# Performance work log

Hardware: AMD Instinct MI355X
Metric: run time of the kernel (lower is better)

The kernel has to match this reference:

```python
import jax, jax.numpy as jnp
import numpy as np

B, T, C = 2, 2048, 1024
H = 16
HS = C // H
EPS = 1e-5


def layernorm(x, g, b):
    mu = jnp.mean(x, axis=-1, keepdims=True)
    var = jnp.var(x, axis=-1, keepdims=True)
    return (x - mu) * jax.lax.rsqrt(var + EPS) * g + b


def setup_inputs() -> dict:
    key = jax.random.key(0)
    ks = jax.random.split(key, 12)
    s_in = 1.0 / np.sqrt(C)
    s_ff = 1.0 / np.sqrt(4 * C)
    return {
        "x": jax.random.normal(ks[0], (B, T, C), jnp.float32),
        "Wq": jax.random.normal(ks[1], (H, C, HS), jnp.float32) * s_in,
        "Wk": jax.random.normal(ks[2], (H, C, HS), jnp.float32) * s_in,
        "Wv": jax.random.normal(ks[3], (H, C, HS), jnp.float32) * s_in,
        "Wo": jax.random.normal(ks[4], (C, C), jnp.float32) * s_in,
        "bo": jnp.zeros((C,), jnp.float32),
        "W1": jax.random.normal(ks[5], (C, 4 * C), jnp.float32) * s_in,
        "b1": jnp.zeros((4 * C,), jnp.float32),
        "W2": jax.random.normal(ks[6], (4 * C, C), jnp.float32) * s_ff,
        "b2": jnp.zeros((C,), jnp.float32),
        "g1": jnp.ones((C,), jnp.float32),
        "be1": jnp.zeros((C,), jnp.float32),
        "g2": jnp.ones((C,), jnp.float32),
        "be2": jnp.zeros((C,), jnp.float32),
    }


def reference(x, Wq, Wk, Wv, Wo, bo, W1, b1, W2, b2, g1, be1, g2, be2):
    # x: [B,T,C]. Dropout is identity (eval mode).
    x = layernorm(x, g1, be1)
    # --- multi-head causal self-attention (per-source: scale by C**-0.5, NOT head_size) ---
    q = jnp.einsum("btc,hcd->bhtd", x, Wq)
    k = jnp.einsum("btc,hcd->bhtd", x, Wk)
    v = jnp.einsum("btc,hcd->bhtd", x, Wv)
    scores = jnp.einsum("bhtd,bhsd->bhts", q, k) * (C ** -0.5)  # [B,H,T,T]
    causal = jnp.tril(jnp.ones((T, T), bool))
    scores = jnp.where(causal, scores, -jnp.inf)
    wei = jax.nn.softmax(scores, axis=-1)
    attn = jnp.einsum("bhts,bhsd->bhtd", wei, v)
    attn = attn.transpose(0, 2, 1, 3).reshape(B, T, C)  # concat heads on last dim
    sa = attn @ Wo + bo
    x = x + sa
    # --- MLP with second pre-op LayerNorm ---
    x = layernorm(x, g2, be2)
    h = jax.nn.relu(x @ W1 + b1)
    x = x + (h @ W2 + b2)
    return x
```

## Files before the change

### kernel.cpp

```cpp
#include <hip/hip_runtime.h>
#include <hip/hip_bf16.h>
#include <math.h>

#define B_ 2
#define T_ 2048
#define C_ 1024
#define H_ 16
#define HS_ 64
#define N_ROWS (B_*T_)
#define MB (1024*1024)

typedef __attribute__((ext_vector_type(8))) short bf16x8;
typedef __attribute__((ext_vector_type(8))) unsigned short u16x8;
typedef __attribute__((ext_vector_type(4))) float floatx4;

static __device__ __forceinline__ unsigned short f2bf(float f) {
  union { float f; unsigned u; } v; v.f = f;
  unsigned r = v.u + 0x7fff + ((v.u >> 16) & 1);
  return (unsigned short)(r >> 16);
}
static __device__ __forceinline__ float bf2f(unsigned short s) {
  union { unsigned u; float f; } v; v.u = ((unsigned)s) << 16;
  return v.f;
}

__global__ __launch_bounds__(256) void ln_kernel(
    const float* __restrict__ x, const float* __restrict__ g,
    const float* __restrict__ b, unsigned short* __restrict__ outb)
{
  const int row = blockIdx.x;
  const int tid = threadIdx.x;
  const float* xr = x + (size_t)row * C_;
  float4 xv = *reinterpret_cast<const float4*>(xr + tid * 4);
  float s  = xv.x + xv.y + xv.z + xv.w;
  float ss = xv.x*xv.x + xv.y*xv.y + xv.z*xv.z + xv.w*xv.w;
  #pragma unroll
  for (int off = 32; off > 0; off >>= 1) {
    s  += __shfl_down(s, off, 64);
    ss += __shfl_down(ss, off, 64);
  }
  __shared__ float rs[4], rss[4];
  __shared__ float smu, srstd;
  if ((tid & 63) == 0) { rs[tid >> 6] = s; rss[tid >> 6] = ss; }
  __syncthreads();
  if (tid == 0) {
    float S  = rs[0] + rs[1] + rs[2] + rs[3];
    float SS = rss[0] + rss[1] + rss[2] + rss[3];
    float mu  = S * (1.0f / C_);
    float var = SS * (1.0f / C_) - mu * mu;
    smu = mu; srstd = rsqrtf(var + 1e-5f);
  }
  __syncthreads();
  const float mu = smu, rstd = srstd;
  float4 gv = *reinterpret_cast<const float4*>(g + tid * 4);
  float4 bv = *reinterpret_cast<const float4*>(b + tid * 4);
  union { unsigned long long ll; unsigned short s[4]; } o;
  o.s[0] = f2bf((xv.x - mu) * rstd * gv.x + bv.x);
  o.s[1] = f2bf((xv.y - mu) * rstd * gv.y + bv.y);
  o.s[2] = f2bf((xv.z - mu) * rstd * gv.z + bv.z);
  o.s[3] = f2bf((xv.w - mu) * rstd * gv.w + bv.w);
  *reinterpret_cast<unsigned long long*>(outb + (size_t)row * C_ + tid * 4) = o.ll;
}

__global__ __launch_bounds__(256) void transpose_cast(
    const float* __restrict__ in, unsigned short* __restrict__ out, int R, int Cc)
{
  __shared__ float tile[32][33];
  const int bz = blockIdx.z;
  in  += (size_t)bz * R * Cc;
  out += (size_t)bz * R * Cc;
  const int tx = threadIdx.x & 31;
  const int ty = threadIdx.x >> 5;
  const int c0 = blockIdx.x * 32, r0 = blockIdx.y * 32;
  #pragma unroll
  for (int j = 0; j < 4; ++j)
    tile[ty + j*8][tx] = in[(size_t)(r0 + ty + j*8) * Cc + c0 + tx];
  __syncthreads();
  #pragma unroll
  for (int j = 0; j < 4; ++j)
    out[(size_t)(c0 + ty + j*8) * R + r0 + tx] = f2bf(tile[tx][ty + j*8]);
}

__global__ __launch_bounds__(256) void transpose_cast_qkv(
    const float* __restrict__ Wq, const float* __restrict__ Wk,
    const float* __restrict__ Wv, unsigned short* __restrict__ out)
{
  __shared__ float tile[32][33];
  const int z = blockIdx.z;
  const int which = z >> 4, h = z & 15;
  const float* in = (which == 0 ? Wq : which == 1 ? Wk : Wv) + (size_t)h * C_ * HS_;
  unsigned short* dst = out + (size_t)z * C_ * HS_;
  const int tx = threadIdx.x & 31;
  const int ty = threadIdx.x >> 5;
  const int c0 = blockIdx.x * 32, r0 = blockIdx.y * 32;
  #pragma unroll
  for (int j = 0; j < 4; ++j)
    tile[ty + j*8][tx] = in[(size_t)(r0 + ty + j*8) * HS_ + c0 + tx];
  __syncthreads();
  #pragma unroll
  for (int j = 0; j < 4; ++j)
    dst[(size_t)(c0 + ty + j*8) * C_ + r0 + tx] = f2bf(tile[tx][ty + j*8]);
}

template<int TNB, bool OUTBF16, bool RELU, bool HASB, bool HASRES>
__global__ __launch_bounds__(256) void gemm_bf16(
    const unsigned short* __restrict__ A,
    const unsigned short* __restrict__ Bt,
    const float* __restrict__ bias,
    const unsigned short* __restrict__ res,
    void* __restrict__ Cout,
    int M, int N, int K)
{
  constexpr int NT = TNB / 32;
  constexpr int WN = TNB / 2;
  __shared__ unsigned short As[2][128 * 32];
  __shared__ unsigned short Bs[2][TNB * 32];
  const int tid  = threadIdx.x;
  const int lane = tid & 63;
  const int wave = tid >> 6;
  const int wm = wave & 1, wn = wave >> 1;
  const int m0 = blockIdx.x * 128, n0 = blockIdx.y * TNB;

  const int lrow = lane >> 2;
  const int lcol = (lane & 3) * 8;
  const int fr = lane & 15;
  const int fq = lane >> 4;

  floatx4 acc[4][NT] = {};

  const unsigned short* Aw = A  + (size_t)m0 * K;
  const unsigned short* Bw = Bt + (size_t)n0 * K;

  for (int k0 = 0; k0 < K; k0 += 64) {
    __syncthreads();
    #pragma unroll
    for (int half = 0; half < 2; ++half) {
      #pragma unroll
      for (int i = 0; i < 2; ++i) {
        const int rbase = i * 64 + wave * 16;
        const unsigned short* gp =
            Aw + (size_t)(rbase + lrow) * K + k0 + half * 32 + lcol;
        __builtin_amdgcn_global_load_lds(
            (const __attribute__((address_space(1))) void*)gp,
            (__attribute__((address_space(3))) void*)(As[half] + rbase * 32),
            16, 0, 0);
      }
      #pragma unroll
      for (int i = 0; i < TNB / 64; ++i) {
        const int rbase = i * 64 + wave * 16;
        const unsigned short* gp =
            Bw + (size_t)(rbase + lrow) * K + k0 + half * 32 + lcol;
        __builtin_amdgcn_global_load_lds(
            (const __attribute__((address_space(1))) void*)gp,
            (__attribute__((address_space(3))) void*)(Bs[half] + rbase * 32),
            16, 0, 0);
      }
    }
    __syncthreads();

    #pragma unroll
    for (int half = 0; half < 2; ++half) {
      bf16x8 af[4], bfr[NT];
      #pragma unroll
      for (int t = 0; t < 4; ++t)
        af[t]  = *reinterpret_cast<const bf16x8*>(
            As[half] + (wm*64 + t*16 + fr)*32 + fq*8);
      #pragma unroll
      for (int t = 0; t < NT; ++t)
        bfr[t] = *reinterpret_cast<const bf16x8*>(
            Bs[half] + (wn*WN + t*16 + fr)*32 + fq*8);
      #pragma unroll
      for (int mt = 0; mt < 4; ++mt)
        #pragma unroll
        for (int nt = 0; nt < NT; ++nt)
          acc[mt][nt] = __builtin_amdgcn_mfma_f32_16x16x32_bf16(
              af[mt], bfr[nt], acc[mt][nt], 0, 0, 0);
    }
  }

  #pragma unroll
  for (int nt = 0; nt < NT; ++nt) {
    const int col = n0 + wn*WN + nt*16 + fr;
    const float bv = HASB ? bias[col] : 0.0f;
    #pragma unroll
    for (int mt = 0; mt < 4; ++mt) {
      #pragma unroll
      for (int r = 0; r < 4; ++r) {
        const int row = m0 + wm*64 + mt*16 + fq*4 + r;
        float v = acc[mt][nt][r] + bv;
        if (RELU) v = v > 0.0f ? v : 0.0f;
        if (HASRES) v += bf2f(res[(size_t)row * N + col]);
        if (OUTBF16) ((unsigned short*)Cout)[(size_t)row * N + col] = f2bf(v);
        else         ((float*)Cout)[(size_t)row * N + col] = v;
      }
    }
  }
}

template<int TNB, int SPLITS>
__global__ __launch_bounds__(256) void gemm_splitk(
    const unsigned short* __restrict__ A,
    const unsigned short* __restrict__ Bt,
    unsigned short* __restrict__ Cpart,
    int M, int N, int Kfull)
{
  constexpr int NT = TNB / 32;
  constexpr int WN = TNB / 2;
  __shared__ unsigned short As[2][128 * 32];
  __shared__ unsigned short Bs[2][TNB * 32];
  const int tid  = threadIdx.x;
  const int lane = tid & 63;
  const int wave = tid >> 6;
  const int wm = wave & 1, wn = wave >> 1;
  const int m0 = blockIdx.x * 128, n0 = blockIdx.y * TNB;
  const int z  = blockIdx.z;
  const int Kh = Kfull / SPLITS;

  const int lrow = lane >> 2;
  const int lcol = (lane & 3) * 8;
  const int fr = lane & 15;
  const int fq = lane >> 4;

  floatx4 acc[4][NT] = {};

  const unsigned short* Aw = A  + (size_t)m0 * Kfull + (size_t)z * Kh;
  const unsigned short* Bw = Bt + (size_t)n0 * Kfull + (size_t)z * Kh;
  unsigned short* Cw = Cpart + (size_t)z * M * N;

  for (int k0 = 0; k0 < Kh; k0 += 64) {
    __syncthreads();
    #pragma unroll
    for (int half = 0; half < 2; ++half) {
      #pragma unroll
      for (int i = 0; i < 2; ++i) {
        const int rbase = i * 64 + wave * 16;
        const unsigned short* gp =
            Aw + (size_t)(rbase + lrow) * Kfull + k0 + half * 32 + lcol;
        __builtin_amdgcn_global_load_lds(
            (const __attribute__((address_space(1))) void*)gp,
            (__attribute__((address_space(3))) void*)(As[half] + rbase * 32),
            16, 0, 0);
      }
      #pragma unroll
      for (int i = 0; i < TNB / 64; ++i) {
        const int rbase = i * 64 + wave * 16;
        const unsigned short* gp =
            Bw + (size_t)(rbase + lrow) * Kfull + k0 + half * 32 + lcol;
        __builtin_amdgcn_global_load_lds(
            (const __attribute__((address_space(1))) void*)gp,
            (__attribute__((address_space(3))) void*)(Bs[half] + rbase * 32),
            16, 0, 0);
      }
    }
    __syncthreads();

    #pragma unroll
    for (int half = 0; half < 2; ++half) {
      bf16x8 af[4], bfr[NT];
      #pragma unroll
      for (int t = 0; t < 4; ++t)
        af[t]  = *reinterpret_cast<const bf16x8*>(
            As[half] + (wm*64 + t*16 + fr)*32 + fq*8);
      #pragma unroll
      for (int t = 0; t < NT; ++t)
        bfr[t] = *reinterpret_cast<const bf16x8*>(
            Bs[half] + (wn*WN + t*16 + fr)*32 + fq*8);
      #pragma unroll
      for (int mt = 0; mt < 4; ++mt)
        #pragma unroll
        for (int nt = 0; nt < NT; ++nt)
          acc[mt][nt] = __builtin_amdgcn_mfma_f32_16x16x32_bf16(
              af[mt], bfr[nt], acc[mt][nt], 0, 0, 0);
    }
  }

  #pragma unroll
  for (int nt = 0; nt < NT; ++nt) {
    const int col = n0 + wn*WN + nt*16 + fr;
    #pragma unroll
    for (int mt = 0; mt < 4; ++mt)
      #pragma unroll
      for (int r = 0; r < 4; ++r) {
        const int row = m0 + wm*64 + mt*16 + fq*4 + r;
        Cw[(size_t)row * N + col] = f2bf(acc[mt][nt][r]);
      }
  }
}

template<int SPLITS>
__global__ __launch_bounds__(256) void splitk_reduce(
    const unsigned short* __restrict__ p,
    const float* __restrict__ bias, const unsigned short* __restrict__ res,
    float* __restrict__ out)
{
  const size_t i = ((size_t)blockIdx.x * 256 + threadIdx.x) * 4;
  const size_t MN = (size_t)N_ROWS * C_;
  float4 bv = *reinterpret_cast<const float4*>(bias + (i & (size_t)(C_ - 1)));
  float acc[4] = {bv.x, bv.y, bv.z, bv.w};
  {
    const unsigned short* rp = res + i;
    #pragma unroll
    for (int j = 0; j < 4; ++j) acc[j] += bf2f(rp[j]);
  }
  #pragma unroll
  for (int z = 0; z < SPLITS; ++z) {
    const unsigned short* pp = p + (size_t)z * MN + i;
    #pragma unroll
    for (int j = 0; j < 4; ++j) acc[j] += bf2f(pp[j]);
  }
  float4 o; o.x = acc[0]; o.y = acc[1]; o.z = acc[2]; o.w = acc[3];
  *reinterpret_cast<float4*>(out + i) = o;
}

__global__ __launch_bounds__(256) void v_transpose(
    const unsigned short* __restrict__ qkv, unsigned short* __restrict__ vt)
{
  __shared__ __align__(16) unsigned short sT[64][72];
  const int st = blockIdx.x;
  const int bh = blockIdx.y;
  const int b = bh >> 4, h = bh & 15;
  const int t = threadIdx.x;
  const int r = t >> 2, c0 = (t & 3) * 16;
  const unsigned short* src =
      qkv + (size_t)(b * T_ + st * 64 + r) * 3072 + 2048 + h * 64 + c0;
  *(u16x8*)&sT[r][c0]     = *(const u16x8*)src;
  *(u16x8*)&sT[r][c0 + 8] = *(const u16x8*)(src + 8);
  __syncthreads();
  const int d = t >> 2, sc = (t & 3) * 16;
  unsigned short v[16];
  #pragma unroll
  for (int j = 0; j < 16; ++j) v[j] = sT[sc + j][d];
  unsigned short* dst = vt + ((size_t)bh * 64 + d) * (size_t)T_ + st * 64 + sc;
  *(uint4*)dst       = *(uint4*)&v[0];
  *(uint4*)(dst + 8) = *(uint4*)&v[8];
}

__global__ __launch_bounds__(256, 3) void attn_mfma(
    const unsigned short* __restrict__ qkv,
    const unsigned short* __restrict__ vt,
    unsigned short* __restrict__ out)
{
  const int bh = blockIdx.x;
  const int qt = (int)(gridDim.y - 1) - (int)blockIdx.y;
  const int b = bh >> 4, h = bh & 15;
  const int tid = threadIdx.x;
  const int w = tid >> 6;
  const int lane = tid & 63;
  const int l15 = lane & 15, fq = lane >> 4;
  const int t0 = qt * 64;
  const int q_row = t0 + w * 16 + l15;

  __shared__ __align__(16) unsigned short sK [128][72];
  __shared__ __align__(16) unsigned short sVt[64][136];
  __shared__ __align__(16) unsigned short sP [64][136];

  const float c1 = 1.4426950408889634f / 32.0f;

  bf16x8 aq[2];
  {
    const unsigned short* qp = qkv + (size_t)(b*T_ + q_row)*3072 + h*HS_ + fq*8;
    aq[0] = *(const bf16x8*)qp;
    aq[1] = *(const bf16x8*)(qp + 32);
  }

  const int nks = (qt >> 1) + 1;

  const int kr = tid >> 1, kc = (tid & 1) * 32;
  const int vr = tid >> 2, vc = (tid & 3) * 32;
  const unsigned short* kp0 =
      qkv + (size_t)(b*T_ + kr)*3072 + C_ + h*HS_ + kc;
  const unsigned short* vp0 =
      vt + ((size_t)bh*64 + vr)*(size_t)T_ + vc;

  u16x8 kg0, kg1, kg2, kg3, vg0, vg1, vg2, vg3;
  kg0 = *(const u16x8*)kp0;      kg1 = *(const u16x8*)(kp0 + 8);
  kg2 = *(const u16x8*)(kp0+16); kg3 = *(const u16x8*)(kp0 + 24);
  vg0 = *(const u16x8*)vp0;      vg1 = *(const u16x8*)(vp0 + 8);
  vg2 = *(const u16x8*)(vp0+16); vg3 = *(const u16x8*)(vp0 + 24);
  *(u16x8*)&sK [kr][kc]      = kg0; *(u16x8*)&sK [kr][kc + 8]  = kg1;
  *(u16x8*)&sK [kr][kc + 16] = kg2; *(u16x8*)&sK [kr][kc + 24] = kg3;
  *(u16x8*)&sVt[vr][vc]      = vg0; *(u16x8*)&sVt[vr][vc + 8]  = vg1;
  *(u16x8*)&sVt[vr][vc + 16] = vg2; *(u16x8*)&sVt[vr][vc + 24] = vg3;

  floatx4 oacc[4] = {};
  float m_s = -3.0e38f, l_s = 0.0f;

  #pragma unroll 1
  for (int ks = 0; ks < nks; ++ks) {
    asm volatile("s_waitcnt lgkmcnt(0)" ::: "memory");
    __builtin_amdgcn_s_barrier();

    if (ks + 1 < nks) {
      const unsigned short* kp = kp0 + (size_t)(ks + 1) * (128 * 3072);
      kg0 = *(const u16x8*)kp;        kg1 = *(const u16x8*)(kp + 8);
      kg2 = *(const u16x8*)(kp + 16); kg3 = *(const u16x8*)(kp + 24);
      const unsigned short* vp = vp0 + (ks + 1) * 128;
      vg0 = *(const u16x8*)vp;        vg1 = *(const u16x8*)(vp + 8);
      vg2 = *(const u16x8*)(vp + 16); vg3 = *(const u16x8*)(vp + 24);
    }

    floatx4 stacc[8] = {};
    __builtin_amdgcn_s_setprio(1);
    #pragma unroll
    for (int st = 0; st < 8; ++st) {
      bf16x8 ka = *(const bf16x8*)&sK[st*16 + l15][fq*8];
      bf16x8 kb = *(const bf16x8*)&sK[st*16 + l15][32 + fq*8];
      stacc[st] = __builtin_amdgcn_mfma_f32_16x16x32_bf16(ka, aq[0], stacc[st], 0, 0, 0);
      stacc[st] = __builtin_amdgcn_mfma_f32_16x16x32_bf16(kb, aq[1], stacc[st], 0, 0, 0);
    }
    __builtin_amdgcn_s_setprio(0);

    if (ks == nks - 1) {
      const int sbase = ks*128 + fq*4;
      #pragma unroll
      for (int st = 0; st < 8; ++st)
        #pragma unroll
        for (int r = 0; r < 4; ++r)
          if (sbase + st*16 + r > q_row) stacc[st][r] = -3.0e38f;
    }

    float mx = -3.0e38f;
    #pragma unroll
    for (int st = 0; st < 8; ++st)
      #pragma unroll
      for (int r = 0; r < 4; ++r) mx = fmaxf(mx, stacc[st][r]);
    mx = fmaxf(mx, __shfl_xor(mx, 16, 64));
    mx = fmaxf(mx, __shfl_xor(mx, 32, 64));

    float mnew;
    if (__all((mx - m_s) * c1 <= 8.0f)) {
      mnew = m_s;
    } else {
      mnew = fmaxf(m_s, mx);
      const float alpha = __builtin_amdgcn_exp2f((m_s - mnew) * c1);
      #pragma unroll
      for (int r = 0; r < 4; ++r) {
        const float ar = __shfl(alpha, fq*4 + r, 64);
        #pragma unroll
        for (int dt = 0; dt < 4; ++dt) oacc[dt][r] *= ar;
      }
      l_s *= alpha;
      m_s = mnew;
    }

    const float mc = mnew * c1;
    float sum = 0.0f;
    #pragma unroll
    for (int st = 0; st < 8; ++st) {
      unsigned pu[4];
      #pragma unroll
      for (int r = 0; r < 4; ++r) {
        const float p = __builtin_amdgcn_exp2f(stacc[st][r] * c1 - mc);
        sum += p;
        union { float f; unsigned u; } cv; cv.f = p;
        pu[r] = cv.u + 0x8000u;
      }
      const unsigned lo = __builtin_amdgcn_perm(pu[1], pu[0], 0x07060302u);
      const unsigned hi = __builtin_amdgcn_perm(pu[3], pu[2], 0x07060302u);
      *(unsigned long long*)&sP[w*16 + l15][st*16 + fq*4] =
          ((unsigned long long)hi << 32) | lo;
    }
    sum += __shfl_xor(sum, 16, 64);
    sum += __shfl_xor(sum, 32, 64);
    l_s += sum;

    __builtin_amdgcn_s_setprio(1);
    #pragma unroll
    for (int c = 0; c < 4; ++c) {
      bf16x8 ap = *(const bf16x8*)&sP[w*16 + l15][c*32 + fq*8];
      #pragma unroll
      for (int dt = 0; dt < 4; ++dt) {
        bf16x8 bv = *(const bf16x8*)&sVt[dt*16 + l15][c*32 + fq*8];
        oacc[dt] = __builtin_amdgcn_mfma_f32_16x16x32_bf16(ap, bv, oacc[dt], 0, 0, 0);
      }
    }
    __builtin_amdgcn_s_setprio(0);

    asm volatile("s_waitcnt lgkmcnt(0)" ::: "memory");
    __builtin_amdgcn_s_barrier();
    if (ks + 1 < nks) {
      *(u16x8*)&sK [kr][kc]      = kg0; *(u16x8*)&sK [kr][kc + 8]  = kg1;
      *(u16x8*)&sK [kr][kc + 16] = kg2; *(u16x8*)&sK [kr][kc + 24] = kg3;
      *(u16x8*)&sVt[vr][vc]      = vg0; *(u16x8*)&sVt[vr][vc + 8]  = vg1;
      *(u16x8*)&sVt[vr][vc + 16] = vg2; *(u16x8*)&sVt[vr][vc + 24] = vg3;
    }
  }

  #pragma unroll
  for (int r = 0; r < 4; ++r) {
    const float il = 1.0f / __shfl(l_s, fq*4 + r, 64);
    const int q = t0 + w*16 + fq*4 + r;
    #pragma unroll
    for (int dt = 0; dt < 4; ++dt)
      out[(size_t)(b*T_ + q)*C_ + h*HS_ + dt*16 + l15] = f2bf(oacc[dt][r] * il);
  }
}

extern "C" void kernel_launch(void* const* d_in, const int* in_sizes, int n_in,
                              void* d_out, int out_size, void* d_ws, size_t ws_size,
                              hipStream_t stream)
{
  const float* x   = (const float*)d_in[0];
  const float* Wq  = (const float*)d_in[1];
  const float* Wk  = (const float*)d_in[2];
  const float* Wv  = (const float*)d_in[3];
  const float* Wo  = (const float*)d_in[4];
  const float* bo  = (const float*)d_in[5];
  const float* W1  = (const float*)d_in[6];
  const float* b1  = (const float*)d_in[7];
  const float* W2  = (const float*)d_in[8];
  const float* b2  = (const float*)d_in[9];
  const float* g1  = (const float*)d_in[10];
  const float* be1 = (const float*)d_in[11];
  const float* g2  = (const float*)d_in[12];
  const float* be2 = (const float*)d_in[13];
  float* out = (float*)d_out;

  char* ws = (char*)d_ws;
  unsigned short* BtQKV = (unsigned short*)(ws + (size_t) 0*MB);
  unsigned short* BtWo  = (unsigned short*)(ws + (size_t) 6*MB);
  unsigned short* BtW1  = (unsigned short*)(ws + (size_t) 8*MB);
  unsigned short* BtW2  = (unsigned short*)(ws + (size_t)16*MB);
  unsigned short* lnb   = (unsigned short*)(ws + (size_t)24*MB);
  unsigned short* qkvb  = (unsigned short*)(ws + (size_t)32*MB);
  unsigned short* vtb   = (unsigned short*)(ws + (size_t)56*MB);
  unsigned short* attnb = (unsigned short*)(ws + (size_t)64*MB);
  float*          x2    = (float*)         (ws + (size_t)32*MB);
  unsigned short* hb    = (unsigned short*)(ws + (size_t)32*MB);
  unsigned short* pk4   = (unsigned short*)(ws + (size_t)64*MB);

  dim3 blk(256);

  transpose_cast_qkv<<<dim3(HS_/32, C_/32, 3*H_), blk, 0, stream>>>(Wq, Wk, Wv, BtQKV);
  transpose_cast<<<dim3(C_/32,  C_/32, 1),  blk, 0, stream>>>(Wo, BtWo, C_, C_);
  transpose_cast<<<dim3(4*C_/32,C_/32, 1),  blk, 0, stream>>>(W1, BtW1, C_, 4*C_);
  transpose_cast<<<dim3(C_/32,4*C_/32, 1),  blk, 0, stream>>>(W2, BtW2, 4*C_, C_);

  ln_kernel<<<dim3(N_ROWS), blk, 0, stream>>>(x, g1, be1, lnb);

  gemm_bf16<128,true,false,false,false><<<dim3(N_ROWS/128, 3072/128), blk, 0, stream>>>(
      lnb, BtQKV, nullptr, nullptr, qkvb, N_ROWS, 3072, C_);

  v_transpose<<<dim3(T_/64, B_*H_), blk, 0, stream>>>(qkvb, vtb);

  attn_mfma<<<dim3(B_*H_, T_/64), blk, 0, stream>>>(qkvb, vtb, attnb);

  gemm_bf16<64,false,false,true,true><<<dim3(N_ROWS/128, C_/64), blk, 0, stream>>>(
      attnb, BtWo, bo, lnb, x2, N_ROWS, C_, C_);

  ln_kernel<<<dim3(N_ROWS), blk, 0, stream>>>(x2, g2, be2, lnb);

  gemm_bf16<128,true,true,true,false><<<dim3(N_ROWS/128, 4*C_/128), blk, 0, stream>>>(
      lnb, BtW1, b1, nullptr, hb, N_ROWS, 4*C_, C_);

  gemm_splitk<128,4><<<dim3(N_ROWS/128, C_/128, 4), blk, 0, stream>>>(
      hb, BtW2, pk4, N_ROWS, C_, 4*C_);

  splitk_reduce<4><<<dim3((N_ROWS * C_) / (256 * 4)), blk, 0, stream>>>(
      pk4, b2, lnb, out);
}
```

Before: 355.9 us.

## Double-buffer GEMM LDS tiles and remap workgroups across XCDs

```diff
diff --git a/kernel.cpp b/kernel.cpp
--- a/kernel.cpp
+++ b/kernel.cpp
@@ -113,13 +113,19 @@
 {
   constexpr int NT = TNB / 32;
   constexpr int WN = TNB / 2;
-  __shared__ unsigned short As[2][128 * 32];
-  __shared__ unsigned short Bs[2][TNB * 32];
+  constexpr int LOADS = 4 + 2 * (TNB / 64);
+  __shared__ unsigned short As[2][2][128 * 32];
+  __shared__ unsigned short Bs[2][2][TNB * 32];
   const int tid  = threadIdx.x;
   const int lane = tid & 63;
   const int wave = tid >> 6;
   const int wm = wave & 1, wn = wave >> 1;
-  const int m0 = blockIdx.x * 128, n0 = blockIdx.y * TNB;
+
+  const int nbx = gridDim.x;
+  const int nwg = nbx * gridDim.y;
+  int bid = blockIdx.y * nbx + blockIdx.x;
+  bid = (bid & 7) * (nwg >> 3) + (bid >> 3);
+  const int m0 = (bid % nbx) * 128, n0 = (bid / nbx) * TNB;
 
   const int lrow = lane >> 2;
   const int lcol = (lane & 3) * 8;
@@ -131,8 +137,7 @@
   const unsigned short* Aw = A  + (size_t)m0 * K;
   const unsigned short* Bw = Bt + (size_t)n0 * K;
 
-  for (int k0 = 0; k0 < K; k0 += 64) {
-    __syncthreads();
+  auto STAGE = [&](int bb, int k0) {
     #pragma unroll
     for (int half = 0; half < 2; ++half) {
       #pragma unroll
@@ -142,7 +147,7 @@
             Aw + (size_t)(rbase + lrow) * K + k0 + half * 32 + lcol;
         __builtin_amdgcn_global_load_lds(
             (const __attribute__((address_space(1))) void*)gp,
-            (__attribute__((address_space(3))) void*)(As[half] + rbase * 32),
+            (__attribute__((address_space(3))) void*)(As[bb][half] + rbase * 32),
             16, 0, 0);
       }
       #pragma unroll
@@ -152,23 +157,24 @@
             Bw + (size_t)(rbase + lrow) * K + k0 + half * 32 + lcol;
         __builtin_amdgcn_global_load_lds(
             (const __attribute__((address_space(1))) void*)gp,
-            (__attribute__((address_space(3))) void*)(Bs[half] + rbase * 32),
+            (__attribute__((address_space(3))) void*)(Bs[bb][half] + rbase * 32),
             16, 0, 0);
       }
     }
-    __syncthreads();
-
+  };
+
+  auto COMPUTE = [&](int bb) {
     #pragma unroll
     for (int half = 0; half < 2; ++half) {
       bf16x8 af[4], bfr[NT];
       #pragma unroll
       for (int t = 0; t < 4; ++t)
         af[t]  = *reinterpret_cast<const bf16x8*>(
-            As[half] + (wm*64 + t*16 + fr)*32 + fq*8);
+            As[bb][half] + (wm*64 + t*16 + fr)*32 + fq*8);
       #pragma unroll
       for (int t = 0; t < NT; ++t)
         bfr[t] = *reinterpret_cast<const bf16x8*>(
-            Bs[half] + (wn*WN + t*16 + fr)*32 + fq*8);
+            Bs[bb][half] + (wn*WN + t*16 + fr)*32 + fq*8);
       #pragma unroll
       for (int mt = 0; mt < 4; ++mt)
         #pragma unroll
@@ -176,7 +182,21 @@
           acc[mt][nt] = __builtin_amdgcn_mfma_f32_16x16x32_bf16(
               af[mt], bfr[nt], acc[mt][nt], 0, 0, 0);
     }
-  }
+  };
+
+  STAGE(0, 0);
+  int bb = 0;
+  for (int k0 = 64; k0 < K; k0 += 64) {
+    STAGE(bb ^ 1, k0);
+    asm volatile("s_waitcnt vmcnt(%0)" :: "n"(LOADS) : "memory");
+    __builtin_amdgcn_s_barrier();
+    COMPUTE(bb);
+    __builtin_amdgcn_s_barrier();
+    bb ^= 1;
+  }
+  asm volatile("s_waitcnt vmcnt(0)" ::: "memory");
+  __builtin_amdgcn_s_barrier();
+  COMPUTE(bb);
 
   #pragma unroll
   for (int nt = 0; nt < NT; ++nt) {
@@ -206,15 +226,21 @@
 {
   constexpr int NT = TNB / 32;
   constexpr int WN = TNB / 2;
-  __shared__ unsigned short As[2][128 * 32];
-  __shared__ unsigned short Bs[2][TNB * 32];
+  constexpr int LOADS = 4 + 2 * (TNB / 64);
+  __shared__ unsigned short As[2][2][128 * 32];
+  __shared__ unsigned short Bs[2][2][TNB * 32];
   const int tid  = threadIdx.x;
   const int lane = tid & 63;
   const int wave = tid >> 6;
   const int wm = wave & 1, wn = wave >> 1;
-  const int m0 = blockIdx.x * 128, n0 = blockIdx.y * TNB;
   const int z  = blockIdx.z;
   const int Kh = Kfull / SPLITS;
+
+  const int nbx = gridDim.x;
+  const int nwg = nbx * gridDim.y;
+  int bid = blockIdx.y * nbx + blockIdx.x;
+  bid = (bid & 7) * (nwg >> 3) + (bid >> 3);
+  const int m0 = (bid % nbx) * 128, n0 = (bid / nbx) * TNB;
 
   const int lrow = lane >> 2;
   const int lcol = (lane & 3) * 8;
@@ -227,8 +253,7 @@
   const unsigned short* Bw = Bt + (size_t)n0 * Kfull + (size_t)z * Kh;
   unsigned short* Cw = Cpart + (size_t)z * M * N;
 
-  for (int k0 = 0; k0 < Kh; k0 += 64) {
-    __syncthreads();
+  auto STAGE = [&](int bb, int k0) {
     #pragma unroll
     for (int half = 0; half < 2; ++half) {
       #pragma unroll
@@ -238,7 +263,7 @@
             Aw + (size_t)(rbase + lrow) * Kfull + k0 + half * 32 + lcol;
         __builtin_amdgcn_global_load_lds(
             (const __attribute__((address_space(1))) void*)gp,
-            (__attribute__((address_space(3))) void*)(As[half] + rbase * 32),
+            (__attribute__((address_space(3))) void*)(As[bb][half] + rbase * 32),
             16, 0, 0);
       }
       #pragma unroll
@@ -248,23 +273,24 @@
             Bw + (size_t)(rbase + lrow) * Kfull + k0 + half * 32 + lcol;
         __builtin_amdgcn_global_load_lds(
             (const __attribute__((address_space(1))) void*)gp,
-            (__attribute__((address_space(3))) void*)(Bs[half] + rbase * 32),
+            (__attribute__((address_space(3))) void*)(Bs[bb][half] + rbase * 32),
             16, 0, 0);
       }
     }
-    __syncthreads();
-
+  };
+
+  auto COMPUTE = [&](int bb) {
     #pragma unroll
     for (int half = 0; half < 2; ++half) {
       bf16x8 af[4], bfr[NT];
       #pragma unroll
       for (int t = 0; t < 4; ++t)
         af[t]  = *reinterpret_cast<const bf16x8*>(
-            As[half] + (wm*64 + t*16 + fr)*32 + fq*8);
+            As[bb][half] + (wm*64 + t*16 + fr)*32 + fq*8);
       #pragma unroll
       for (int t = 0; t < NT; ++t)
         bfr[t] = *reinterpret_cast<const bf16x8*>(
-            Bs[half] + (wn*WN + t*16 + fr)*32 + fq*8);
+            Bs[bb][half] + (wn*WN + t*16 + fr)*32 + fq*8);
       #pragma unroll
       for (int mt = 0; mt < 4; ++mt)
         #pragma unroll
@@ -272,7 +298,21 @@
           acc[mt][nt] = __builtin_amdgcn_mfma_f32_16x16x32_bf16(
               af[mt], bfr[nt], acc[mt][nt], 0, 0, 0);
     }
-  }
+  };
+
+  STAGE(0, 0);
+  int bb = 0;
+  for (int k0 = 64; k0 < Kh; k0 += 64) {
+    STAGE(bb ^ 1, k0);
+    asm volatile("s_waitcnt vmcnt(%0)" :: "n"(LOADS) : "memory");
+    __builtin_amdgcn_s_barrier();
+    COMPUTE(bb);
+    __builtin_amdgcn_s_barrier();
+    bb ^= 1;
+  }
+  asm volatile("s_waitcnt vmcnt(0)" ::: "memory");
+  __builtin_amdgcn_s_barrier();
+  COMPUTE(bb);
 
   #pragma unroll
   for (int nt = 0; nt < NT; ++nt) {
```

Result: slower. 363.3 us (+2.1%).
